# Kernel optimization log

Hardware: AMD Instinct MI355X
Metric: run time of the kernel (lower is better)

The kernel has to match this reference:

```python
import jax, jax.numpy as jnp
import numpy as np

ORDER = 2
HIDDEN = 64
INPUT_SIZE = 2
N_NODES = 1024
BATCH = 8
STEPS = 32
GN_EPS = 1e-5


def setup_inputs() -> dict:
    key = jax.random.key(0)
    ks = jax.random.split(key, 8)
    c_gate_in = INPUT_SIZE + HIDDEN            # channels of concat([x, h]) fed to gate convs
    n_supp = 2 * ORDER                          # fwd/bwd row-normalized adj + (order-1) powers each
    c_conv = (n_supp + 1) * c_gate_in           # include_self=True adds the identity (self) block

    def w(k, shape, fan_in):
        s = 1.0 / np.sqrt(fan_in)
        return jax.random.uniform(k, shape, jnp.float32, -s, s)

    return {
        "x":   jax.random.normal(ks[0], (BATCH, INPUT_SIZE, N_NODES, STEPS), jnp.float32),
        "adj": jax.random.uniform(ks[1], (N_NODES, N_NODES), jnp.float32),
        "h0":  jax.random.normal(ks[2], (HIDDEN, N_NODES), jnp.float32) / np.sqrt(HIDDEN),
        "Wr": w(ks[3], (HIDDEN, c_conv), c_conv), "br": jnp.zeros((HIDDEN,), jnp.float32),
        "Wu": w(ks[4], (HIDDEN, c_conv), c_conv), "bu": jnp.zeros((HIDDEN,), jnp.float32),
        "Wc": w(ks[5], (HIDDEN, c_conv), c_conv), "bc": jnp.zeros((HIDDEN,), jnp.float32),
        "gamma": jnp.ones((HIDDEN,), jnp.float32), "beta": jnp.zeros((HIDDEN,), jnp.float32),
        "Wo": w(ks[6], (INPUT_SIZE, HIDDEN), HIDDEN), "bo": jnp.zeros((INPUT_SIZE,), jnp.float32),
    }


def _supports(adj, order):
    # SpatialConvOrderK.compute_support_orderK(adj, K, include_self=True)
    fwd = adj / (adj.sum(1, keepdims=True) + 1e-8)
    bwd = adj.T / (adj.T.sum(1, keepdims=True) + 1e-8)
    supp = [fwd, bwd]
    for a in (fwd, bwd):
        ak = a
        for _ in range(order - 1):
            ak = ak @ a.T               # higher-order diffusion; include_self -> keep diagonal
            supp.append(ak)
    return jnp.stack(supp)              # [S, n, n], S = 2*order


def _gconv(z, supp, W, b):
    # order-1 graph conv over precomputed order-K supports, include_self=True
    # z: [b, c, n]; supp: [S, n, n]; torch: einsum('ncvl,wv->ncwl')
    agg = jnp.einsum('bcv,swv->bscw', z, supp)            # [b, S, c, n]
    zc = jnp.concatenate([z[:, None], agg], axis=1)       # [b, S+1, c, n] (self first)
    zc = zc.reshape(z.shape[0], -1, z.shape[2])           # [b, (S+1)*c, n]
    return jnp.einsum('oc,bcn->bon', W, zc) + b[None, :, None]


def _gnorm(h, gamma, beta):
    # GroupNorm(num_groups=1): normalize each sample over (channels, nodes)
    m = h.mean(axis=(1, 2), keepdims=True)
    v = ((h - m) ** 2).mean(axis=(1, 2), keepdims=True)
    return (h - m) * jax.lax.rsqrt(v + GN_EPS) * gamma[None, :, None] + beta[None, :, None]


def reference(x, adj, h0, Wr, br, Wu, bu, Wc, bc, gamma, beta, Wo, bo):
    supp = _supports(adj, ORDER)
    b, _, n, _ = x.shape
    h = jnp.broadcast_to(h0[None], (b, HIDDEN, n))
    xs = jnp.moveaxis(x, -1, 0)                           # [steps, b, c_in, n]

    def step(h, xt):
        zg = jnp.concatenate([xt, h], axis=1)             # [b, c_in+hidden, n]
        r = jax.nn.sigmoid(_gconv(zg, supp, Wr, br))      # reset gate
        u = jax.nn.sigmoid(_gconv(zg, supp, Wu, bu))      # update gate
        zc = jnp.concatenate([xt, r * h], axis=1)
        c = jnp.tanh(_gconv(zc, supp, Wc, bc))            # candidate
        hn = _gnorm(u * h + (1.0 - u) * c, gamma, beta)   # norm applied post-cell (h[layer] = norm(...))
        x_hat = jnp.einsum('oc,bcn->bon', Wo, hn) + bo[None, :, None]  # first_stage 1x1 conv
        return hn, (x_hat, hn)

    _, (imps, hs) = jax.lax.scan(step, h, xs)
    imputations = jnp.moveaxis(imps, 0, -1)               # [b, input_size, n, steps]
    states = jnp.moveaxis(hs, 0, -1)[None]                # [n_layers=1, b, hidden, n, steps]
    return imputations, states
```

## Files before the change

### kernel.cpp

```cpp
#include <hip/hip_runtime.h>
#include <math.h>

#define NN 1024
#define HID 64
#define CIN 2
#define BB 8
#define TT 32
#define CG 66
#define NBC 528
#define K2 384
#define GN_EPS 1e-5f
#define LDAP 72

typedef __attribute__((ext_vector_type(8))) short short8v;
typedef __attribute__((ext_vector_type(4))) float float4v;

#define GLD16(gp, lp) __builtin_amdgcn_global_load_lds( \
    (const __attribute__((address_space(1))) void*)(gp), \
    (__attribute__((address_space(3))) void*)(lp), 16, 0, 0)

__device__ __forceinline__ unsigned short f2b(float v) {
    union { float f; unsigned int u; } a; a.f = v;
    unsigned int r = a.u + 0x7FFFu + ((a.u >> 16) & 1u);
    return (unsigned short)(r >> 16);
}
__device__ __forceinline__ float b2f(unsigned short b) {
    union { unsigned int u; float f; } a; a.u = ((unsigned int)b) << 16;
    return a.f;
}
__device__ __forceinline__ float sigmoidf_(float v) { return 1.f / (1.f + __expf(-v)); }

__device__ __forceinline__ float wave_reduce_sum(float v) {
    #pragma unroll
    for (int o = 32; o > 0; o >>= 1) v += __shfl_down(v, o, 64);
    return v;
}


__global__ void rowsum_k(const float* __restrict__ adj, float* __restrict__ rs) {
    int i = blockIdx.x;
    float s = 0.f;
    for (int j = threadIdx.x; j < NN; j += 256) s += adj[(size_t)i * NN + j];
    s = wave_reduce_sum(s);
    __shared__ float sh[4];
    int wid = threadIdx.x >> 6, lid = threadIdx.x & 63;
    if (lid == 0) sh[wid] = s;
    __syncthreads();
    if (threadIdx.x == 0) rs[i] = sh[0] + sh[1] + sh[2] + sh[3];
}

__global__ void colsum_k(const float* __restrict__ adj, float* __restrict__ cpart) {
    int j = (blockIdx.x & 3) * 256 + threadIdx.x;
    int r0 = (blockIdx.x >> 2) * 128;
    float s = 0.f;
    for (int i = 0; i < 128; i++) s += adj[(size_t)(r0 + i) * NN + j];
    cpart[(size_t)(blockIdx.x >> 2) * NN + j] = s;
}

__global__ void fwdb_k(const float* __restrict__ adj, const float* __restrict__ rs,
                       unsigned short* __restrict__ sb) {
    int idx = blockIdx.x * 256 + threadIdx.x;
    int i = idx >> 10;
    sb[idx] = f2b(adj[idx] / (rs[i] + 1e-8f));
}

__global__ void bwdb_k(const float* __restrict__ adj, const float* __restrict__ cpart,
                       unsigned short* __restrict__ sb) {
    __shared__ float tile[32][33];
    int i0 = blockIdx.y * 32, j0 = blockIdx.x * 32;
    int tx = threadIdx.x, ty = threadIdx.y;
    #pragma unroll
    for (int r = ty; r < 32; r += 8)
        tile[r][tx] = adj[(size_t)(j0 + r) * NN + i0 + tx];
    __syncthreads();
    #pragma unroll
    for (int r = ty; r < 32; r += 8) {
        int i = i0 + r;
        float cs = 0.f;
        #pragma unroll
        for (int c = 0; c < 8; c++) cs += cpart[(size_t)c * NN + i];
        sb[(size_t)i * NN + j0 + tx] = f2b(tile[tx][r] / (cs + 1e-8f));
    }
}

__global__ __launch_bounds__(256) void suppk_mfma(const unsigned short* __restrict__ sb,
                                                  unsigned short* __restrict__ outb) {
    int z = blockIdx.z;
    const unsigned short* A = sb + (size_t)z * NN * NN;
    unsigned short* D = outb + (size_t)z * NN * NN;
    __shared__ unsigned short lA[128 * LDAP];
    __shared__ unsigned short lB[64 * LDAP];
    int tid = threadIdx.x;
    int m0 = blockIdx.x * 128, n0 = blockIdx.y * 64;
    int lane = tid & 63, wave = tid >> 6;
    int wm = wave >> 1, wn = wave & 1;
    float4v acc[4][2];
    #pragma unroll
    for (int i = 0; i < 4; i++)
        #pragma unroll
        for (int j = 0; j < 2; j++) acc[i][j] = (float4v){0.f, 0.f, 0.f, 0.f};
    int lrow = lane & 15, lk8 = (lane >> 4) * 8;
    for (int k0 = 0; k0 < NN; k0 += 64) {
        #pragma unroll
        for (int s = 0; s < 4; s++) {
            int slot = tid + s * 256;
            int r = slot >> 3, kg = slot & 7;
            *(short8v*)(lA + r * LDAP + kg * 8) =
                *(const short8v*)(A + (size_t)(m0 + r) * NN + k0 + kg * 8);
        }
        #pragma unroll
        for (int s = 0; s < 2; s++) {
            int slot = tid + s * 256;
            int r = slot >> 3, kg = slot & 7;
            *(short8v*)(lB + r * LDAP + kg * 8) =
                *(const short8v*)(A + (size_t)(n0 + r) * NN + k0 + kg * 8);
        }
        __syncthreads();
        #pragma unroll
        for (int kk = 0; kk < 2; kk++) {
            short8v af[4], bf[2];
            #pragma unroll
            for (int i = 0; i < 4; i++)
                af[i] = *(const short8v*)(lA + (wm * 64 + i * 16 + lrow) * LDAP + kk * 32 + lk8);
            #pragma unroll
            for (int j = 0; j < 2; j++)
                bf[j] = *(const short8v*)(lB + (wn * 32 + j * 16 + lrow) * LDAP + kk * 32 + lk8);
            #pragma unroll
            for (int i = 0; i < 4; i++)
                #pragma unroll
                for (int j = 0; j < 2; j++)
                    acc[i][j] = __builtin_amdgcn_mfma_f32_16x16x32_bf16(af[i], bf[j], acc[i][j], 0, 0, 0);
        }
        __syncthreads();
    }
    int col = lane & 15, q4 = (lane >> 4) * 4;
    #pragma unroll
    for (int i = 0; i < 4; i++)
        #pragma unroll
        for (int j = 0; j < 2; j++) {
            int n = n0 + wn * 32 + j * 16 + col;
            #pragma unroll
            for (int r = 0; r < 4; r++) {
                int mm = m0 + wm * 64 + i * 16 + q4 + r;
                D[(size_t)mm * NN + n] = f2b(acc[i][j][r]);
            }
        }
}

__global__ void wconv_k(const float* __restrict__ Wr, const float* __restrict__ Wu,
                        const float* __restrict__ Wc, unsigned short* __restrict__ Wb,
                        unsigned short* __restrict__ Wcb) {
    int idx = blockIdx.x * 256 + threadIdx.x;
    int row = idx / K2, j = idx - row * K2;
    float v = 0.f;
    if (j < 330) {
        int q = j / CG, rr = j - q * CG;
        int chan = q * CG + (rr < HID ? rr + CIN : rr - HID);
        if (row < 64) v = Wr[row * 330 + chan];
        else if (row < 128) v = Wu[(row - 64) * 330 + chan];
        else v = Wc[(row - 128) * 330 + chan];
    }
    if (row < 128) Wb[row * K2 + j] = f2b(v);
    else Wcb[(row - 128) * K2 + j] = f2b(v);
}

__global__ void zeroz_k(unsigned short* __restrict__ z) {
    size_t i = ((size_t)blockIdx.x * 256 + threadIdx.x) * 8;
    *(short8v*)(z + i) = (short8v){0, 0, 0, 0, 0, 0, 0, 0};
}

__global__ void init_k(const float* __restrict__ x, const float* __restrict__ h0,
                       float* __restrict__ h, unsigned short* __restrict__ Z2g,
                       unsigned short* __restrict__ Z2c, unsigned short* __restrict__ Abfg,
                       unsigned short* __restrict__ Abfc) {
    int m = blockIdx.x * 256 + threadIdx.x;
    int b = m >> 10, n = m & 1023;
    for (int c = 0; c < HID; c++) {
        float v = h0[(c << 10) + n];
        h[(size_t)m * HID + c] = v;
        unsigned short hv = f2b(v);
        Z2g[(size_t)m * K2 + c] = hv;
        Abfg[(((size_t)(b * CG + c)) << 10) | n] = hv;
    }
    for (int o = 0; o < CIN; o++) {
        float xv = x[((((size_t)(b * CIN + o)) << 10) + n) * TT];
        unsigned short xb = f2b(xv);
        Z2g[(size_t)m * K2 + HID + o] = xb;
        Z2c[(size_t)m * K2 + HID + o] = xb;
        Abfg[(((size_t)(b * CG + HID + o)) << 10) | n] = xb;
        Abfc[(((size_t)(b * CG + HID + o)) << 10) | n] = xb;
    }
}


__global__ __launch_bounds__(256) void agg2_k(const unsigned short* __restrict__ S,
                                              const unsigned short* __restrict__ Abf,
                                              unsigned short* __restrict__ Z2) {
    __shared__ __align__(16) unsigned short lA[3][64 * 64];
    __shared__ __align__(16) unsigned short lB[3][64 * 64];
    int tid = threadIdx.x;
    int lin = blockIdx.y * 9 + blockIdx.x;
    int swz = (lin & 7) * 72 + (lin >> 3);
    int c0 = (swz % 9) * 64;
    int m0 = (swz / 9) * 64;
    int lane = tid & 63, wave = tid >> 6;
    int wm = wave >> 1, wn = wave & 1;
    float4v acc[2][2];
    #pragma unroll
    for (int i = 0; i < 2; i++)
        #pragma unroll
        for (int j = 0; j < 2; j++) acc[i][j] = (float4v){0.f, 0.f, 0.f, 0.f};
    int lrow = lane & 15, hi = lane >> 4;

    auto stage = [&](unsigned short* bufA, unsigned short* bufB, int k0) {
        #pragma unroll
        for (int i = 0; i < 2; i++) {
            int cid = (i * 4 + wave) * 64 + lane;
            int r = cid >> 3, sz = cid & 7;
            GLD16(S + (size_t)(m0 + r) * NN + k0 + ((sz ^ (r & 7)) << 3),
                  bufA + (i * 4 + wave) * 512);
        }
        #pragma unroll
        for (int i = 0; i < 2; i++) {
            int cid = (i * 4 + wave) * 64 + lane;
            int r = cid >> 3, sz = cid & 7;
            GLD16(Abf + (((size_t)(c0 + r)) << 10) + k0 + ((sz ^ (r & 7)) << 3),
                  bufB + (i * 4 + wave) * 512);
        }
    };

    unsigned short *a0 = lA[0], *a1 = lA[1], *a2 = lA[2];
    unsigned short *b0 = lB[0], *b1 = lB[1], *b2 = lB[2];
    stage(a0, b0, 0);
    stage(a1, b1, 64);
    for (int kt = 0; kt < 16; kt++) {
        if (kt < 15) asm volatile("s_waitcnt vmcnt(4)" ::: "memory");
        else         asm volatile("s_waitcnt vmcnt(0)" ::: "memory");
        __builtin_amdgcn_s_barrier();
        asm volatile("" ::: "memory");
        if (kt < 14) stage(a2, b2, (kt + 2) * 64);
        #pragma unroll
        for (int kk = 0; kk < 2; kk++) {
            int cb = kk * 4 + hi;
            short8v af[2], bf[2];
            #pragma unroll
            for (int i = 0; i < 2; i++) {
                int lr = wm * 32 + i * 16 + lrow;
                af[i] = *(const short8v*)(a0 + lr * 64 + ((cb ^ (lr & 7)) << 3));
            }
            #pragma unroll
            for (int j = 0; j < 2; j++) {
                int lr = wn * 32 + j * 16 + lrow;
                bf[j] = *(const short8v*)(b0 + lr * 64 + ((cb ^ (lr & 7)) << 3));
            }
            #pragma unroll
            for (int i = 0; i < 2; i++)
                #pragma unroll
                for (int j = 0; j < 2; j++)
                    acc[i][j] = __builtin_amdgcn_mfma_f32_16x16x32_bf16(af[i], bf[j], acc[i][j], 0, 0, 0);
        }
        { unsigned short* t = a0; a0 = a1; a1 = a2; a2 = t; }
        { unsigned short* t = b0; b0 = b1; b1 = b2; b2 = t; }
    }
    int col = lane & 15, q4 = (lane >> 4) * 4;
    int s_idx = m0 >> 10;
    int nb0 = (m0 & 1023) + wm * 32;
    #pragma unroll
    for (int j = 0; j < 2; j++) {
        int bc = c0 + wn * 32 + j * 16 + col;
        if (bc < NBC) {
            int b = bc / CG;
            int rr = bc - b * CG;
            size_t zcol = (size_t)CG + s_idx * CG + rr;
            #pragma unroll
            for (int i = 0; i < 2; i++) {
                int nb = nb0 + i * 16 + q4;
                #pragma unroll
                for (int r = 0; r < 4; r++)
                    Z2[((size_t)((b << 10) | (nb + r))) * K2 + zcol] = f2b(acc[i][j][r]);
            }
        }
    }
}

__global__ __launch_bounds__(256) void gates_k2(const unsigned short* __restrict__ Z2g,
                                                const unsigned short* __restrict__ Wb,
                                                const float* __restrict__ br,
                                                const float* __restrict__ bu,
                                                const float* __restrict__ h,
                                                float* __restrict__ u,
                                                unsigned short* __restrict__ Z2c,
                                                unsigned short* __restrict__ Abfc) {
    __shared__ __align__(16) unsigned short lA[3][64 * 64];
    __shared__ __align__(16) unsigned short lB[3][64 * 64];
    int tid = threadIdx.x;
    int m0 = blockIdx.x * 64;
    int isU = blockIdx.y;
    const unsigned short* W = Wb + (size_t)isU * 64 * K2;
    int lane = tid & 63, wave = tid >> 6;
    int wm = wave >> 1, wn = wave & 1;
    float4v acc[2][2];
    #pragma unroll
    for (int i = 0; i < 2; i++)
        #pragma unroll
        for (int j = 0; j < 2; j++) acc[i][j] = (float4v){0.f, 0.f, 0.f, 0.f};
    int lrow = lane & 15, hi = lane >> 4;

    auto stage = [&](unsigned short* bufA, unsigned short* bufB, int k0) {
        #pragma unroll
        for (int i = 0; i < 2; i++) {
            int cid = (i * 4 + wave) * 64 + lane;
            int r = cid >> 3, sz = cid & 7;
            GLD16(Z2g + (size_t)(m0 + r) * K2 + k0 + ((sz ^ (r & 7)) << 3),
                  bufA + (i * 4 + wave) * 512);
        }
        #pragma unroll
        for (int i = 0; i < 2; i++) {
            int cid = (i * 4 + wave) * 64 + lane;
            int r = cid >> 3, sz = cid & 7;
            GLD16(W + (size_t)r * K2 + k0 + ((sz ^ (r & 7)) << 3),
                  bufB + (i * 4 + wave) * 512);
        }
    };

    unsigned short *a0 = lA[0], *a1 = lA[1], *a2 = lA[2];
    unsigned short *b0 = lB[0], *b1 = lB[1], *b2 = lB[2];
    stage(a0, b0, 0);
    stage(a1, b1, 64);
    for (int kt = 0; kt < 6; kt++) {
        if (kt < 5) asm volatile("s_waitcnt vmcnt(4)" ::: "memory");
        else        asm volatile("s_waitcnt vmcnt(0)" ::: "memory");
        __builtin_amdgcn_s_barrier();
        asm volatile("" ::: "memory");
        if (kt < 4) stage(a2, b2, (kt + 2) * 64);
        #pragma unroll
        for (int kk = 0; kk < 2; kk++) {
            int cb = kk * 4 + hi;
            short8v af[2], bf[2];
            #pragma unroll
            for (int i = 0; i < 2; i++) {
                int lr = wm * 32 + i * 16 + lrow;
                af[i] = *(const short8v*)(a0 + lr * 64 + ((cb ^ (lr & 7)) << 3));
            }
            #pragma unroll
            for (int j = 0; j < 2; j++) {
                int lr = wn * 32 + j * 16 + lrow;
                bf[j] = *(const short8v*)(b0 + lr * 64 + ((cb ^ (lr & 7)) << 3));
            }
            #pragma unroll
            for (int i = 0; i < 2; i++)
                #pragma unroll
                for (int j = 0; j < 2; j++)
                    acc[i][j] = __builtin_amdgcn_mfma_f32_16x16x32_bf16(af[i], bf[j], acc[i][j], 0, 0, 0);
        }
        { unsigned short* t = a0; a0 = a1; a1 = a2; a2 = t; }
        { unsigned short* t = b0; b0 = b1; b1 = b2; b2 = t; }
    }
    int col = lane & 15, q4 = (lane >> 4) * 4;
    #pragma unroll
    for (int i = 0; i < 2; i++)
        #pragma unroll
        for (int j = 0; j < 2; j++) {
            int oo = wn * 32 + j * 16 + col;
            float bias = isU ? bu[oo] : br[oo];
            #pragma unroll
            for (int r = 0; r < 4; r++) {
                int m = m0 + wm * 32 + i * 16 + q4 + r;
                float g = sigmoidf_(acc[i][j][r] + bias);
                if (isU) {
                    u[(size_t)m * HID + oo] = g;
                } else {
                    float rh = g * h[(size_t)m * HID + oo];
                    unsigned short hv = f2b(rh);
                    Z2c[(size_t)m * K2 + oo] = hv;
                    int b = m >> 10, n = m & 1023;
                    Abfc[(((size_t)(b * CG + oo)) << 10) | n] = hv;
                }
            }
        }
}

__global__ __launch_bounds__(256) void cand_k2(const unsigned short* __restrict__ Z2c,
                                               const unsigned short* __restrict__ Wcb,
                                               const float* __restrict__ bcv,
                                               const float* __restrict__ u,
                                               const float* __restrict__ h,
                                               float* __restrict__ hraw,
                                               float* __restrict__ stats2, int t) {
    __shared__ __align__(16) unsigned short lA[3][32 * 64];
    __shared__ __align__(16) unsigned short lB[3][64 * 64];
    int tid = threadIdx.x;
    int m0 = blockIdx.x * 32;
    int lane = tid & 63, wave = tid >> 6;
    int wm = wave >> 1, wn = wave & 1;
    float4v acc[2];
    acc[0] = (float4v){0.f, 0.f, 0.f, 0.f};
    acc[1] = (float4v){0.f, 0.f, 0.f, 0.f};
    int lrow = lane & 15, hi = lane >> 4;

    auto stage = [&](unsigned short* bufA, unsigned short* bufB, int k0) {
        {
            int cid = wave * 64 + lane;
            int r = cid >> 3, sz = cid & 7;
            GLD16(Z2c + (size_t)(m0 + r) * K2 + k0 + ((sz ^ (r & 7)) << 3),
                  bufA + wave * 512);
        }
        #pragma unroll
        for (int i = 0; i < 2; i++) {
            int cid = (i * 4 + wave) * 64 + lane;
            int r = cid >> 3, sz = cid & 7;
            GLD16(Wcb + (size_t)r * K2 + k0 + ((sz ^ (r & 7)) << 3),
                  bufB + (i * 4 + wave) * 512);
        }
    };

    unsigned short *a0 = lA[0], *a1 = lA[1], *a2 = lA[2];
    unsigned short *b0 = lB[0], *b1 = lB[1], *b2 = lB[2];
    stage(a0, b0, 0);
    stage(a1, b1, 64);
    for (int kt = 0; kt < 6; kt++) {
        if (kt < 5) asm volatile("s_waitcnt vmcnt(3)" ::: "memory");
        else        asm volatile("s_waitcnt vmcnt(0)" ::: "memory");
        __builtin_amdgcn_s_barrier();
        asm volatile("" ::: "memory");
        if (kt < 4) stage(a2, b2, (kt + 2) * 64);
        #pragma unroll
        for (int kk = 0; kk < 2; kk++) {
            int cb = kk * 4 + hi;
            short8v af, bf[2];
            {
                int lr = wm * 16 + lrow;
                af = *(const short8v*)(a0 + lr * 64 + ((cb ^ (lr & 7)) << 3));
            }
            #pragma unroll
            for (int j = 0; j < 2; j++) {
                int lr = wn * 32 + j * 16 + lrow;
                bf[j] = *(const short8v*)(b0 + lr * 64 + ((cb ^ (lr & 7)) << 3));
            }
            #pragma unroll
            for (int j = 0; j < 2; j++)
                acc[j] = __builtin_amdgcn_mfma_f32_16x16x32_bf16(af, bf[j], acc[j], 0, 0, 0);
        }
        { unsigned short* t = a0; a0 = a1; a1 = a2; a2 = t; }
        { unsigned short* t = b0; b0 = b1; b1 = b2; b2 = t; }
    }
    int col = lane & 15, q4 = (lane >> 4) * 4;
    float ls = 0.f, ls2 = 0.f;
    #pragma unroll
    for (int j = 0; j < 2; j++) {
        int oo = wn * 32 + j * 16 + col;
        float bias = bcv[oo];
        #pragma unroll
        for (int r = 0; r < 4; r++) {
            int m = m0 + wm * 16 + q4 + r;
            float cv = tanhf(acc[j][r] + bias);
            float uv = u[(size_t)m * HID + oo];
            float hv = h[(size_t)m * HID + oo];
            float hr = uv * hv + (1.f - uv) * cv;
            hraw[(size_t)m * HID + oo] = hr;
            ls += hr;
            ls2 = fmaf(hr, hr, ls2);
        }
    }
    ls = wave_reduce_sum(ls);
    ls2 = wave_reduce_sum(ls2);
    __shared__ float sred[8];
    if (lane == 0) { sred[wave] = ls; sred[4 + wave] = ls2; }
    __syncthreads();
    if (tid == 0) {
        float S = sred[0] + sred[1] + sred[2] + sred[3];
        float S2 = sred[4] + sred[5] + sred[6] + sred[7];
        int b = blockIdx.x >> 5, slot = blockIdx.x & 31;
        float* dst = stats2 + (((size_t)t * BB + b) * 32 + slot) * 2;
        dst[0] = S;
        dst[1] = S2;
    }
}

__global__ __launch_bounds__(256) void apply_k2(const float* __restrict__ hraw,
                                                const float* __restrict__ stats2,
                                                const float* __restrict__ gamma,
                                                const float* __restrict__ beta,
                                                const float* __restrict__ Wo,
                                                const float* __restrict__ bo,
                                                const float* __restrict__ x,
                                                float* __restrict__ h,
                                                unsigned short* __restrict__ Z2g,
                                                unsigned short* __restrict__ Z2c,
                                                unsigned short* __restrict__ Abfg,
                                                unsigned short* __restrict__ Abfc,
                                                unsigned short* __restrict__ hseq8,
                                                float* __restrict__ iseq, int t) {
    int gid = blockIdx.x * 256 + threadIdx.x;
    int m = gid >> 3, q = gid & 7;
    int b = m >> 10, n = m & 1023;
    const float* st = stats2 + ((size_t)t * BB + b) * 64;
    float S = 0.f, S2 = 0.f;
    #pragma unroll
    for (int i = 0; i < 16; i++) {
        float4 p4 = *(const float4*)&st[i * 4];
        S += p4.x + p4.z;
        S2 += p4.y + p4.w;
    }
    float mean = S * (1.f / 65536.f);
    float rstd = rsqrtf(S2 * (1.f / 65536.f) - mean * mean + GN_EPS);
    bool more = (t < TT - 1);
    int c0 = q * 8;
    float v[8];
    unsigned short hb[8];
    #pragma unroll
    for (int k = 0; k < 8; k += 4) {
        float4 r4 = *(const float4*)&hraw[(size_t)m * HID + c0 + k];
        v[k + 0] = (r4.x - mean) * rstd * gamma[c0 + k + 0] + beta[c0 + k + 0];
        v[k + 1] = (r4.y - mean) * rstd * gamma[c0 + k + 1] + beta[c0 + k + 1];
        v[k + 2] = (r4.z - mean) * rstd * gamma[c0 + k + 2] + beta[c0 + k + 2];
        v[k + 3] = (r4.w - mean) * rstd * gamma[c0 + k + 3] + beta[c0 + k + 3];
    }
    float acc0 = 0.f, acc1 = 0.f;
    #pragma unroll
    for (int k = 0; k < 8; k++) {
        acc0 = fmaf(Wo[c0 + k], v[k], acc0);
        acc1 = fmaf(Wo[HID + c0 + k], v[k], acc1);
        hb[k] = f2b(v[k]);
    }
    short8v h8;
    #pragma unroll
    for (int k = 0; k < 8; k++) h8[k] = (short)hb[k];
    size_t hsbase = ((size_t)(t & 7) * 8192 + m) * HID + c0;
    *(short8v*)&hseq8[hsbase] = h8;
    if (more) {
        #pragma unroll
        for (int k = 0; k < 8; k += 4)
            *(float4*)&h[(size_t)m * HID + c0 + k] = make_float4(v[k], v[k + 1], v[k + 2], v[k + 3]);
        *(short8v*)&Z2g[(size_t)m * K2 + c0] = h8;
        #pragma unroll
        for (int k = 0; k < 8; k++)
            Abfg[(((size_t)(b * CG + c0 + k)) << 10) | n] = hb[k];
    }
    acc0 += __shfl_xor(acc0, 1, 64); acc0 += __shfl_xor(acc0, 2, 64); acc0 += __shfl_xor(acc0, 4, 64);
    acc1 += __shfl_xor(acc1, 1, 64); acc1 += __shfl_xor(acc1, 2, 64); acc1 += __shfl_xor(acc1, 4, 64);
    if (q == 0) {
        iseq[((size_t)t * 8192 + m) * 2 + 0] = acc0 + bo[0];
        iseq[((size_t)t * 8192 + m) * 2 + 1] = acc1 + bo[1];
        if (more) {
            #pragma unroll
            for (int o = 0; o < CIN; o++) {
                float xv = x[((((size_t)(b * CIN + o)) << 10) + n) * TT + t + 1];
                unsigned short xb = f2b(xv);
                Z2g[(size_t)m * K2 + HID + o] = xb;
                Z2c[(size_t)m * K2 + HID + o] = xb;
                Abfg[(((size_t)(b * CG + HID + o)) << 10) | n] = xb;
                Abfc[(((size_t)(b * CG + HID + o)) << 10) | n] = xb;
            }
        }
    }
}

__global__ __launch_bounds__(256) void strans_k(const unsigned short* __restrict__ hseq8,
                                                float* __restrict__ outS, int t0) {
    __shared__ unsigned short lt[8 * 576];
    int tid = threadIdx.x;
    int b = blockIdx.x >> 7;
    int n0 = (blockIdx.x & 127) * 8;
    #pragma unroll
    for (int s = 0; s < 2; s++) {
        int slot = tid + s * 256;
        int tt = slot >> 6, dn = (slot >> 3) & 7, kc = slot & 7;
        short8v vv = *(const short8v*)(hseq8 + ((size_t)tt * 8192 + ((b << 10) | (n0 + dn))) * HID + kc * 8);
        *(short8v*)(lt + tt * 576 + dn * 72 + kc * 8) = vv;
    }
    __syncthreads();
    #pragma unroll
    for (int s = 0; s < 2; s++) {
        int rid = tid + s * 256;
        int c = rid >> 3, dn = rid & 7;
        float f[8];
        #pragma unroll
        for (int tt = 0; tt < 8; tt++) f[tt] = b2f(lt[tt * 576 + dn * 72 + c]);
        float* dst = outS + ((((size_t)(b * HID + c)) << 10) + n0 + dn) * TT + t0;
        *(float4*)&dst[0] = make_float4(f[0], f[1], f[2], f[3]);
        *(float4*)&dst[4] = make_float4(f[4], f[5], f[6], f[7]);
    }
}

__global__ void itrans_k(const float* __restrict__ iseq, float* __restrict__ out) {
    int gid = blockIdx.x * 256 + threadIdx.x;
    int b = gid >> 11, o = (gid >> 10) & 1, n = gid & 1023;
    float f[TT];
    #pragma unroll
    for (int t = 0; t < TT; t++)
        f[t] = iseq[((size_t)t * 8192 + ((b << 10) | n)) * 2 + o];
    float* dst = out + ((((size_t)(b * CIN + o)) << 10) + n) * TT;
    #pragma unroll
    for (int k = 0; k < TT; k += 4)
        *(float4*)&dst[k] = make_float4(f[k], f[k + 1], f[k + 2], f[k + 3]);
}


extern "C" void kernel_launch(void* const* d_in, const int* in_sizes, int n_in,
                              void* d_out, int out_size, void* d_ws, size_t ws_size,
                              hipStream_t stream) {
    const float* x     = (const float*)d_in[0];
    const float* adj   = (const float*)d_in[1];
    const float* h0    = (const float*)d_in[2];
    const float* Wr    = (const float*)d_in[3];
    const float* br    = (const float*)d_in[4];
    const float* Wu    = (const float*)d_in[5];
    const float* bu    = (const float*)d_in[6];
    const float* Wc    = (const float*)d_in[7];
    const float* bcv   = (const float*)d_in[8];
    const float* gamma = (const float*)d_in[9];
    const float* beta  = (const float*)d_in[10];
    const float* Wo    = (const float*)d_in[11];
    const float* bo    = (const float*)d_in[12];
    float* out = (float*)d_out;

    char* p = (char*)d_ws;
    unsigned short* suppb = (unsigned short*)p;  p += (size_t)4 * NN * NN * 2;
    unsigned short* Abfg  = (unsigned short*)p;  p += (size_t)576 * NN * 2;
    unsigned short* Abfc  = (unsigned short*)p;  p += (size_t)576 * NN * 2;
    unsigned short* Z2g   = (unsigned short*)p;  p += (size_t)8192 * K2 * 2;
    unsigned short* Z2c   = (unsigned short*)p;  p += (size_t)8192 * K2 * 2;
    unsigned short* Wb    = (unsigned short*)p;  p += (size_t)128 * K2 * 2;
    unsigned short* Wcb   = (unsigned short*)p;  p += (size_t)64 * K2 * 2;
    float* u     = (float*)p;  p += (size_t)8192 * HID * 4;
    float* h     = (float*)p;  p += (size_t)8192 * HID * 4;
    float* hraw  = (float*)p;  p += (size_t)8192 * HID * 4;
    unsigned short* hseq8 = (unsigned short*)p;  p += (size_t)8 * 8192 * HID * 2;
    float* iseq  = (float*)p;  p += (size_t)TT * 8192 * 2 * 4;
    float* rowsum = (float*)p; p += NN * 4;
    float* cpart  = (float*)p; p += (size_t)8 * NN * 4;
    float* stats2 = (float*)p; p += (size_t)TT * BB * 32 * 2 * 4;

    float* outS = out + (size_t)BB * CIN * NN * TT;

    rowsum_k<<<NN, 256, 0, stream>>>(adj, rowsum);
    colsum_k<<<32, 256, 0, stream>>>(adj, cpart);
    fwdb_k<<<(NN * NN) / 256, 256, 0, stream>>>(adj, rowsum, suppb);
    bwdb_k<<<dim3(32, 32), dim3(32, 8), 0, stream>>>(adj, cpart, suppb + (size_t)NN * NN);
    suppk_mfma<<<dim3(8, 16, 2), 256, 0, stream>>>(suppb, suppb + (size_t)2 * NN * NN);
    wconv_k<<<(192 * K2) / 256, 256, 0, stream>>>(Wr, Wu, Wc, Wb, Wcb);
    zeroz_k<<<(2 * 8192 * K2) / (8 * 256), 256, 0, stream>>>(Z2g);
    init_k<<<8192 / 256, 256, 0, stream>>>(x, h0, h, Z2g, Z2c, Abfg, Abfc);

    for (int t = 0; t < TT; t++) {
        agg2_k<<<dim3(9, 64), 256, 0, stream>>>(suppb, Abfg, Z2g);
        gates_k2<<<dim3(128, 2), 256, 0, stream>>>(Z2g, Wb, br, bu, h, u, Z2c, Abfc);
        agg2_k<<<dim3(9, 64), 256, 0, stream>>>(suppb, Abfc, Z2c);
        cand_k2<<<256, 256, 0, stream>>>(Z2c, Wcb, bcv, u, h, hraw, stats2, t);
        apply_k2<<<256, 256, 0, stream>>>(hraw, stats2, gamma, beta, Wo, bo, x, h,
                                          Z2g, Z2c, Abfg, Abfc, hseq8, iseq, t);
        if ((t & 7) == 7)
            strans_k<<<1024, 256, 0, stream>>>(hseq8, outS, t - 7);
    }
    itrans_k<<<64, 256, 0, stream>>>(iseq, out);
}
```

Measured before the change: 1.642 ms.

## Switch aggregation GEMM to 32x32x16 MFMA with two-wave blocks

```diff
diff --git a/kernel.cpp b/kernel.cpp
--- a/kernel.cpp
+++ b/kernel.cpp
@@ -14,6 +14,7 @@
 
 typedef __attribute__((ext_vector_type(8))) short short8v;
 typedef __attribute__((ext_vector_type(4))) float float4v;
+typedef __attribute__((ext_vector_type(16))) float float16v;
 
 #define GLD16(gp, lp) __builtin_amdgcn_global_load_lds( \
     (const __attribute__((address_space(1))) void*)(gp), \
@@ -193,39 +194,34 @@
 }
 
 
-__global__ __launch_bounds__(256) void agg2_k(const unsigned short* __restrict__ S,
+__global__ __launch_bounds__(128) void agg3_k(const unsigned short* __restrict__ S,
                                               const unsigned short* __restrict__ Abf,
                                               unsigned short* __restrict__ Z2) {
-    __shared__ __align__(16) unsigned short lA[3][64 * 64];
-    __shared__ __align__(16) unsigned short lB[3][64 * 64];
+    __shared__ __align__(16) unsigned short lA[3][4096];
+    __shared__ __align__(16) unsigned short lB[3][4096];
     int tid = threadIdx.x;
     int lin = blockIdx.y * 9 + blockIdx.x;
     int swz = (lin & 7) * 72 + (lin >> 3);
     int c0 = (swz % 9) * 64;
     int m0 = (swz / 9) * 64;
-    int lane = tid & 63, wave = tid >> 6;
-    int wm = wave >> 1, wn = wave & 1;
-    float4v acc[2][2];
+    int lane = tid & 63, wn = tid >> 6;
+    float16v acc[2];
     #pragma unroll
     for (int i = 0; i < 2; i++)
         #pragma unroll
-        for (int j = 0; j < 2; j++) acc[i][j] = (float4v){0.f, 0.f, 0.f, 0.f};
-    int lrow = lane & 15, hi = lane >> 4;
+        for (int r = 0; r < 16; r++) acc[i][r] = 0.f;
+    int l31 = lane & 31, hi5 = lane >> 5;
 
     auto stage = [&](unsigned short* bufA, unsigned short* bufB, int k0) {
         #pragma unroll
-        for (int i = 0; i < 2; i++) {
-            int cid = (i * 4 + wave) * 64 + lane;
+        for (int i = 0; i < 4; i++) {
+            int g = i * 2 + wn;
+            int cid = g * 64 + lane;
             int r = cid >> 3, sz = cid & 7;
             GLD16(S + (size_t)(m0 + r) * NN + k0 + ((sz ^ (r & 7)) << 3),
-                  bufA + (i * 4 + wave) * 512);
-        }
-        #pragma unroll
-        for (int i = 0; i < 2; i++) {
-            int cid = (i * 4 + wave) * 64 + lane;
-            int r = cid >> 3, sz = cid & 7;
+                  bufA + g * 512);
             GLD16(Abf + (((size_t)(c0 + r)) << 10) + k0 + ((sz ^ (r & 7)) << 3),
-                  bufB + (i * 4 + wave) * 512);
+                  bufB + g * 512);
         }
     };
 
@@ -234,52 +230,47 @@
     stage(a0, b0, 0);
     stage(a1, b1, 64);
     for (int kt = 0; kt < 16; kt++) {
-        if (kt < 15) asm volatile("s_waitcnt vmcnt(4)" ::: "memory");
+        if (kt < 15) asm volatile("s_waitcnt vmcnt(8)" ::: "memory");
         else         asm volatile("s_waitcnt vmcnt(0)" ::: "memory");
         __builtin_amdgcn_s_barrier();
         asm volatile("" ::: "memory");
         if (kt < 14) stage(a2, b2, (kt + 2) * 64);
         #pragma unroll
-        for (int kk = 0; kk < 2; kk++) {
-            int cb = kk * 4 + hi;
-            short8v af[2], bf[2];
-            #pragma unroll
-            for (int i = 0; i < 2; i++) {
-                int lr = wm * 32 + i * 16 + lrow;
-                af[i] = *(const short8v*)(a0 + lr * 64 + ((cb ^ (lr & 7)) << 3));
-            }
-            #pragma unroll
-            for (int j = 0; j < 2; j++) {
-                int lr = wn * 32 + j * 16 + lrow;
-                bf[j] = *(const short8v*)(b0 + lr * 64 + ((cb ^ (lr & 7)) << 3));
-            }
-            #pragma unroll
-            for (int i = 0; i < 2; i++)
-                #pragma unroll
-                for (int j = 0; j < 2; j++)
-                    acc[i][j] = __builtin_amdgcn_mfma_f32_16x16x32_bf16(af[i], bf[j], acc[i][j], 0, 0, 0);
+        for (int kk = 0; kk < 4; kk++) {
+            int cb = kk * 2 + hi5;
+            short8v af0, af1, bf;
+            {
+                int lr = l31;
+                af0 = *(const short8v*)(a0 + lr * 64 + ((cb ^ (lr & 7)) << 3));
+            }
+            {
+                int lr = 32 + l31;
+                af1 = *(const short8v*)(a0 + lr * 64 + ((cb ^ (lr & 7)) << 3));
+            }
+            {
+                int lr = wn * 32 + l31;
+                bf = *(const short8v*)(b0 + lr * 64 + ((cb ^ (lr & 7)) << 3));
+            }
+            acc[0] = __builtin_amdgcn_mfma_f32_32x32x16_bf16(af0, bf, acc[0], 0, 0, 0);
+            acc[1] = __builtin_amdgcn_mfma_f32_32x32x16_bf16(af1, bf, acc[1], 0, 0, 0);
         }
         { unsigned short* t = a0; a0 = a1; a1 = a2; a2 = t; }
         { unsigned short* t = b0; b0 = b1; b1 = b2; b2 = t; }
     }
-    int col = lane & 15, q4 = (lane >> 4) * 4;
     int s_idx = m0 >> 10;
-    int nb0 = (m0 & 1023) + wm * 32;
-    #pragma unroll
-    for (int j = 0; j < 2; j++) {
-        int bc = c0 + wn * 32 + j * 16 + col;
-        if (bc < NBC) {
-            int b = bc / CG;
-            int rr = bc - b * CG;
-            size_t zcol = (size_t)CG + s_idx * CG + rr;
-            #pragma unroll
-            for (int i = 0; i < 2; i++) {
-                int nb = nb0 + i * 16 + q4;
-                #pragma unroll
-                for (int r = 0; r < 4; r++)
-                    Z2[((size_t)((b << 10) | (nb + r))) * K2 + zcol] = f2b(acc[i][j][r]);
-            }
-        }
+    int nbase = m0 & 1023;
+    int bc = c0 + wn * 32 + l31;
+    if (bc < NBC) {
+        int b = bc / CG;
+        int rr = bc - b * CG;
+        size_t zcol = (size_t)CG + s_idx * CG + rr;
+        #pragma unroll
+        for (int i = 0; i < 2; i++)
+            #pragma unroll
+            for (int reg = 0; reg < 16; reg++) {
+                int row = i * 32 + (reg & 3) + 8 * (reg >> 2) + 4 * hi5;
+                Z2[((size_t)((b << 10) | (nbase + row))) * K2 + zcol] = f2b(acc[i][reg]);
+            }
     }
 }
 
@@ -441,8 +432,8 @@
             for (int j = 0; j < 2; j++)
                 acc[j] = __builtin_amdgcn_mfma_f32_16x16x32_bf16(af, bf[j], acc[j], 0, 0, 0);
         }
-        { unsigned short* t = a0; a0 = a1; a1 = a2; a2 = t; }
-        { unsigned short* t = b0; b0 = b1; b1 = b2; b2 = t; }
+        { unsigned short* t_ = a0; a0 = a1; a1 = a2; a2 = t_; }
+        { unsigned short* t_ = b0; b0 = b1; b1 = b2; b2 = t_; }
     }
     int col = lane & 15, q4 = (lane >> 4) * 4;
     float ls = 0.f, ls2 = 0.f;
@@ -644,9 +635,9 @@
     init_k<<<8192 / 256, 256, 0, stream>>>(x, h0, h, Z2g, Z2c, Abfg, Abfc);
 
     for (int t = 0; t < TT; t++) {
-        agg2_k<<<dim3(9, 64), 256, 0, stream>>>(suppb, Abfg, Z2g);
+        agg3_k<<<dim3(9, 64), 128, 0, stream>>>(suppb, Abfg, Z2g);
         gates_k2<<<dim3(128, 2), 256, 0, stream>>>(Z2g, Wb, br, bu, h, u, Z2c, Abfc);
-        agg2_k<<<dim3(9, 64), 256, 0, stream>>>(suppb, Abfc, Z2c);
+        agg3_k<<<dim3(9, 64), 128, 0, stream>>>(suppb, Abfc, Z2c);
         cand_k2<<<256, 256, 0, stream>>>(Z2c, Wcb, bcv, u, h, hraw, stats2, t);
         apply_k2<<<256, 256, 0, stream>>>(hraw, stats2, gamma, beta, Wo, bo, x, h,
                                           Z2g, Z2c, Abfg, Abfc, hseq8, iseq, t);
```

Measured after the change: 1.748 ms. +6.4%, slower.
